# Optimization experiments

Measured on AMD Instinct MI355X. Metric: run time of the kernel, lower is better.

## Reference

```python
import jax, jax.numpy as jnp
import numpy as np

T, N, E = 336, 3233, 20000
FEAT, D, H = 14, 64, 128


def setup_inputs() -> dict:
    key = jax.random.key(0)
    ks = jax.random.split(key, 12)
    s = lambda k, shape, fan: jax.random.normal(k, shape, jnp.float32) / np.sqrt(fan)
    return {
        "x": jax.random.normal(ks[0], (T, N, FEAT), jnp.float32),
        "edge_index": jax.random.randint(ks[1], (2, E), 0, N, jnp.int64 if jax.config.jax_enable_x64 else jnp.int32),
        "edge_weight": jax.random.uniform(ks[2], (E,), jnp.float32),
        "W1": s(ks[3], (FEAT, D), FEAT), "b1": jnp.zeros((D,), jnp.float32),
        "W2": s(ks[4], (D, D), D), "b2": jnp.zeros((D,), jnp.float32),
        "county_bias": s(ks[5], (N, D), D),
        "W_ih": s(ks[6], (4 * H, D), D), "W_hh": s(ks[7], (4 * H, H), H),
        "b_ih": jnp.zeros((4 * H,), jnp.float32), "b_hh": jnp.zeros((4 * H,), jnp.float32),
        "Wm1": s(ks[8], (H, H // 2), H), "bm1": jnp.zeros((H // 2,), jnp.float32),
        "Wm2": s(ks[9], (H // 2, 1), H // 2), "bm2": jnp.zeros((1,), jnp.float32),
    }


def _gcn_norm(edge_index, edge_weight, n):
    # PyG GCNConv: add self-loops (weight 1) + symmetric normalization
    loop = jnp.arange(n, dtype=edge_index.dtype)
    src = jnp.concatenate([edge_index[0], loop])
    dst = jnp.concatenate([edge_index[1], loop])
    w = jnp.concatenate([edge_weight, jnp.ones((n,), edge_weight.dtype)])
    deg = jax.ops.segment_sum(w, dst, num_segments=n)
    dis = jnp.where(deg > 0, jax.lax.rsqrt(jnp.where(deg > 0, deg, 1.0)), 0.0)
    return src, dst, dis[src] * w * dis[dst]


def _gcn(h, src, dst, norm, W, b):
    # h: [T,N,Fin] -> [T,N,Fout]; transform then gather-scale-scatter over edges
    hw = jnp.einsum("tnf,fd->tnd", h, W)
    msg = hw[:, src, :] * norm[None, :, None]          # [T,E',Fout]
    out = jnp.zeros_like(hw).at[:, dst, :].add(msg)
    return out + b


def reference(x, edge_index, edge_weight, W1, b1, W2, b2, county_bias,
              W_ih, W_hh, b_ih, b_hh, Wm1, bm1, Wm2, bm2):
    n = x.shape[1]
    src, dst, norm = _gcn_norm(edge_index, edge_weight, n)
    h = jax.nn.relu(_gcn(x, src, dst, norm, W1, b1))
    embeds = _gcn(h, src, dst, norm, W2, b2) + county_bias[None]  # [T,N,D]

    hid = W_hh.shape[1]
    def step(carry, x_t):  # x_t: [N,D]
        hprev, cprev = carry
        g = x_t @ W_ih.T + hprev @ W_hh.T + (b_ih + b_hh)
        i, f, gg, o = jnp.split(g, 4, axis=-1)
        c = jax.nn.sigmoid(f) * cprev + jax.nn.sigmoid(i) * jnp.tanh(gg)
        hh = jax.nn.sigmoid(o) * jnp.tanh(c)
        return (hh, c), None

    init = (jnp.zeros((n, hid), x.dtype), jnp.zeros((n, hid), x.dtype))
    (h_final, _), _ = jax.lax.scan(step, init, embeds)
    z = jax.nn.relu(h_final @ Wm1 + bm1)
    return (z @ Wm2 + bm2)[:, 0]
```

## Files before the change

### kernel.cpp

```cpp
#include <hip/hip_runtime.h>
#include <math.h>


#define T_DIM 336
#define N_DIM 3233
#define E_DIM 20000
#define FEAT  14
#define D_DIM 64
#define H_DIM 128
#define ET    (E_DIM + N_DIM)

typedef _Float16 f16;
typedef _Float16 half8_t __attribute__((ext_vector_type(8)));
typedef float float4_t __attribute__((ext_vector_type(4)));

__device__ __forceinline__ float sigf(float x) {
    return __builtin_amdgcn_rcpf(1.f + exp2f(-1.4426950408889634f * x));
}
__device__ __forceinline__ float tanhfast(float x) {
    return 1.f - 2.f * __builtin_amdgcn_rcpf(1.f + exp2f(2.8853900817779268f * x));
}


__global__ void k_init(int* cnt, int* fill) {
    int i = blockIdx.x * 256 + threadIdx.x;
    if (i < N_DIM) { cnt[i] = 0; fill[i] = 0; }
}

__global__ void k_cnt(const int* __restrict__ ei, int* cnt) {
    int e = blockIdx.x * 256 + threadIdx.x;
    if (e < E_DIM) atomicAdd(&cnt[ei[E_DIM + e]], 1);
}

__global__ void k_scan(const int* __restrict__ cnt, int* __restrict__ rowp) {
    __shared__ int csum[1024];
    int tid = threadIdx.x;
    int base = tid * 4;
    int v[4];
    int s = 0;
    #pragma unroll
    for (int m = 0; m < 4; m++) {
        int idx = base + m;
        int len = (idx < N_DIM) ? (cnt[idx] + 1) : 0;
        v[m] = s; s += len;
    }
    csum[tid] = s;
    __syncthreads();
    for (int off = 1; off < 1024; off <<= 1) {
        int t2 = (tid >= off) ? csum[tid - off] : 0;
        __syncthreads();
        csum[tid] += t2;
        __syncthreads();
    }
    int pre = (tid > 0) ? csum[tid - 1] : 0;
    #pragma unroll
    for (int m = 0; m < 4; m++) {
        int idx = base + m;
        if (idx <= N_DIM) rowp[idx] = pre + v[m];
    }
}

__global__ void k_fill(const int* __restrict__ ei, const int* __restrict__ rowp,
                       int* fill, int* __restrict__ eid) {
    int e = blockIdx.x * 256 + threadIdx.x;
    if (e < ET) {
        int d = (e < E_DIM) ? ei[E_DIM + e] : (e - E_DIM);
        int p = rowp[d] + atomicAdd(&fill[d], 1);
        eid[p] = e;
    }
}

__global__ void k_sortdeg(const float* __restrict__ ew, const int* __restrict__ rowp,
                          int* __restrict__ eid, float* __restrict__ dis) {
    int n = blockIdx.x * 256 + threadIdx.x;
    if (n >= N_DIM) return;
    int p0 = rowp[n], p1 = rowp[n + 1];
    for (int i = p0 + 1; i < p1; i++) {
        int key = eid[i];
        int j = i - 1;
        while (j >= p0 && eid[j] > key) { eid[j + 1] = eid[j]; j--; }
        eid[j + 1] = key;
    }
    float deg = 0.f;
    for (int p = p0; p < p1; p++) {
        int e = eid[p];
        deg += (e < E_DIM) ? ew[e] : 1.0f;
    }
    dis[n] = rsqrtf(deg);
}

__global__ void k_csrmat(const int* __restrict__ ei, const float* __restrict__ ew,
                         const float* __restrict__ dis, const int* __restrict__ rowp,
                         const int* __restrict__ eid, int* __restrict__ csrc,
                         float* __restrict__ cnrm) {
    int n = blockIdx.x * 256 + threadIdx.x;
    if (n >= N_DIM) return;
    float dn = dis[n];
    int p0 = rowp[n], p1 = rowp[n + 1];
    for (int p = p0; p < p1; p++) {
        int e = eid[p];
        int s; float w;
        if (e < E_DIM) { s = ei[e]; w = ew[e]; }
        else           { s = e - E_DIM; w = 1.0f; }
        csrc[p] = s;
        cnrm[p] = dis[s] * w * dn;
    }
}

__global__ void k_wprep(const float* __restrict__ W2, const float* __restrict__ Wih,
                        const float* __restrict__ Whh, f16* __restrict__ wfbuf) {
    int idx = blockIdx.x * 256 + threadIdx.x;
    if (idx >= 8 * 4 * 6 * 64) return;
    int lane = idx & 63;
    int ks = (idx >> 6) % 6;
    int ct = ((idx >> 6) / 6) & 3;
    int wv = (idx >> 6) / 24;
    int q = lane >> 4, r = lane & 15;
    int g = 128 * ct + 16 * wv + r;
    f16* dst = wfbuf + (long)idx * 8;
    if (ks < 2) {
        const float* wir = Wih + (long)g * 64;
        #pragma unroll
        for (int j = 0; j < 8; j++) {
            int k = 32 * ks + 8 * q + j;
            const float* w2r = W2 + (long)k * 64;
            float s = 0.f;
            #pragma unroll 16
            for (int d = 0; d < 64; d++) s += w2r[d] * wir[d];
            dst[j] = (f16)s;
        }
    } else {
        const float* src = Whh + (long)g * 128 + 32 * (ks - 2) + 8 * q;
        #pragma unroll
        for (int j = 0; j < 8; j++) dst[j] = (f16)src[j];
    }
}

__global__ void k_gbias(const float* __restrict__ county, const float* __restrict__ b2,
                        const float* __restrict__ Wih, const float* __restrict__ bih,
                        const float* __restrict__ bhh, float* __restrict__ gbias) {
    long id = (long)blockIdx.x * 256 + threadIdx.x;
    if (id >= (long)N_DIM * 512) return;
    int n = (int)(id >> 9), g = (int)(id & 511);
    const float* wir = Wih + (long)g * 64;
    const float* cn = county + (long)n * 64;
    float s = bih[g] + bhh[g];
    #pragma unroll 16
    for (int d = 0; d < 64; d++) s += (b2[d] + cn[d]) * wir[d];
    gbias[id] = s;
}

__global__ void k_aggx(const float* __restrict__ x, const int* __restrict__ rowp,
                       const int* __restrict__ csrc, const float* __restrict__ cnrm,
                       float* __restrict__ aggX, int tc) {
    int lane = threadIdx.x & 63;
    long wid = ((long)blockIdx.x * 256 + threadIdx.x) >> 6;
    int ntg = (tc + 3) >> 2;
    if (wid >= (long)N_DIM * ntg) return;
    int n = (int)(wid % N_DIM);
    int tg = (int)(wid / N_DIM);
    int j = lane >> 4, d = lane & 15;
    int tj = 4 * tg + j;
    bool live = (d < FEAT) && (tj < tc);
    float acc = 0.f;
    int p0 = rowp[n], p1 = rowp[n + 1];
    for (int p = p0; p < p1; p++) {
        int s = csrc[p];
        float w = cnrm[p];
        if (live) acc += w * x[((long)tj * N_DIM + s) * FEAT + d];
    }
    if (tj < tc) aggX[((long)tj * N_DIM + n) * 16 + d] = acc;
}

__global__ void k_tr1(const float* __restrict__ aggX, const float* __restrict__ W1,
                      const float* __restrict__ b1, f16* __restrict__ h, long rows) {
    int lane = threadIdx.x & 63;
    long wid = ((long)blockIdx.x * 256 + threadIdx.x) >> 6;
    float wc[FEAT];
    #pragma unroll
    for (int k = 0; k < FEAT; k++) wc[k] = W1[k * 64 + lane];
    float bb = b1[lane];
    long r0 = wid * 2;
    if (r0 >= rows) return;
    long r1 = r0 + 1;
    bool has1 = (r1 < rows);
    const float* p0 = aggX + r0 * 16;
    const float* p1 = aggX + (has1 ? r1 : r0) * 16;
    float a0 = bb, a1 = bb;
    #pragma unroll
    for (int k = 0; k < FEAT; k++) { a0 += p0[k] * wc[k]; a1 += p1[k] * wc[k]; }
    h[r0 * 64 + lane] = (f16)fmaxf(a0, 0.f);
    if (has1) h[r1 * 64 + lane] = (f16)fmaxf(a1, 0.f);
}

__global__ void k_agg2(const f16* __restrict__ h, const int* __restrict__ rowp,
                       const int* __restrict__ csrc, const float* __restrict__ cnrm,
                       f16* __restrict__ ah, int tc) {
    int lane = threadIdx.x & 63;
    long wid = ((long)blockIdx.x * 256 + threadIdx.x) >> 6;
    int ntg = (tc + 3) >> 2;
    if (wid >= (long)N_DIM * ntg) return;
    int n = (int)(wid % N_DIM);
    int tg = (int)(wid / N_DIM);
    int tbase = 4 * tg;
    float acc0 = 0.f, acc1 = 0.f, acc2 = 0.f, acc3 = 0.f;
    int p0 = rowp[n], p1 = rowp[n + 1];
    for (int p = p0; p < p1; p++) {
        int s = csrc[p];
        float w = cnrm[p];
        const f16* base = h + ((long)tbase * N_DIM + s) * 64 + lane;
        acc0 += w * (float)base[0];
        if (tbase + 1 < tc) acc1 += w * (float)base[(long)N_DIM * 64];
        if (tbase + 2 < tc) acc2 += w * (float)base[(long)N_DIM * 128];
        if (tbase + 3 < tc) acc3 += w * (float)base[(long)N_DIM * 192];
    }
    f16* dst = ah + ((long)tbase * N_DIM + n) * 64 + lane;
    dst[0] = (f16)acc0;
    if (tbase + 1 < tc) dst[(long)N_DIM * 64] = (f16)acc1;
    if (tbase + 2 < tc) dst[(long)N_DIM * 128] = (f16)acc2;
    if (tbase + 3 < tc) dst[(long)N_DIM * 192] = (f16)acc3;
}

__global__ __attribute__((amdgpu_flat_work_group_size(512, 512), amdgpu_waves_per_eu(2, 2)))
void k_lstm(
    const f16* __restrict__ ah, const f16* __restrict__ wfbuf,
    const float* __restrict__ gbias,
    const float* __restrict__ Wm1, const float* __restrict__ bm1,
    const float* __restrict__ Wm2, const float* __restrict__ bm2,
    float* __restrict__ Hst, float* __restrict__ Cst,
    int tc, int do_init, int do_head, float* __restrict__ out) {
    __shared__ __align__(16) f16   xh[2][16][136];
    __shared__ __align__(16) float hd[16][132];
    __shared__ __align__(16) float zs[16][64];

    int tid = threadIdx.x;
    int wv = tid >> 6, lane = tid & 63, q = lane >> 4, r = lane & 15;
    int nb = blockIdx.x * 16;
    int cnt = min(16, N_DIM - nb);
    int u = 16 * wv + r;

    float4_t wfr[4][6];
    #pragma unroll
    for (int ct = 0; ct < 4; ct++)
        #pragma unroll
        for (int ks = 0; ks < 6; ks++)
            wfr[ct][ks] = *(const float4_t*)&wfbuf[(long)((((wv * 4 + ct) * 6 + ks) << 6) + lane) * 8];
    #pragma unroll
    for (int ct = 0; ct < 4; ct++)
        #pragma unroll
        for (int ks = 0; ks < 6; ks++)
            asm volatile("" : "+v"(wfr[ct][ks]));

    float gb[4][4];
    #pragma unroll
    for (int reg = 0; reg < 4; reg++) {
        int node = 4 * q + reg;
        int gn = nb + node; if (gn >= N_DIM) gn = N_DIM - 1;
        #pragma unroll
        for (int ct = 0; ct < 4; ct++)
            gb[ct][reg] = gbias[(long)gn * 512 + 128 * ct + u];
    }
    #pragma unroll
    for (int ct = 0; ct < 4; ct++)
        #pragma unroll
        for (int reg = 0; reg < 4; reg++)
            asm volatile("" : "+v"(gb[ct][reg]));

    float cv[4], hvv[4];
    #pragma unroll
    for (int reg = 0; reg < 4; reg++) {
        int node = 4 * q + reg;
        bool live = (!do_init) && (node < cnt);
        hvv[reg] = live ? Hst[(long)(nb + node) * H_DIM + u] : 0.f;
        cv[reg]  = live ? Cst[(long)(nb + node) * H_DIM + u] : 0.f;
        xh[0][node][u] = (f16)hvv[reg];
    }

    int xrow = nb + r; if (xrow >= N_DIM) xrow = N_DIM - 1;
    half8_t xa = *(const half8_t*)(ah + (long)xrow * 64 + 8 * q);
    half8_t xb = *(const half8_t*)(ah + (long)xrow * 64 + 32 + 8 * q);

    int buf = 0;
    __syncthreads();

    for (int t = 0; t < tc; t++) {
        half8_t a2 = *(const half8_t*)&xh[buf][r][8 * q];
        half8_t a3 = *(const half8_t*)&xh[buf][r][32 + 8 * q];
        half8_t a4 = *(const half8_t*)&xh[buf][r][64 + 8 * q];
        half8_t a5 = *(const half8_t*)&xh[buf][r][96 + 8 * q];

        float4_t acc[4];
        #pragma unroll
        for (int ct = 0; ct < 4; ct++) {
            acc[ct][0] = gb[ct][0]; acc[ct][1] = gb[ct][1];
            acc[ct][2] = gb[ct][2]; acc[ct][3] = gb[ct][3];
        }
        #pragma unroll
        for (int ct = 0; ct < 4; ct++)
            acc[ct] = __builtin_amdgcn_mfma_f32_16x16x32_f16(xa, __builtin_bit_cast(half8_t, wfr[ct][0]), acc[ct], 0, 0, 0);
        #pragma unroll
        for (int ct = 0; ct < 4; ct++)
            acc[ct] = __builtin_amdgcn_mfma_f32_16x16x32_f16(xb, __builtin_bit_cast(half8_t, wfr[ct][1]), acc[ct], 0, 0, 0);

        int tn = (t + 1 < tc) ? t + 1 : t;
        const f16* xp = ah + ((long)tn * N_DIM + xrow) * 64;
        xa = *(const half8_t*)(xp + 8 * q);
        xb = *(const half8_t*)(xp + 32 + 8 * q);

        #pragma unroll
        for (int ct = 0; ct < 4; ct++)
            acc[ct] = __builtin_amdgcn_mfma_f32_16x16x32_f16(a2, __builtin_bit_cast(half8_t, wfr[ct][2]), acc[ct], 0, 0, 0);
        #pragma unroll
        for (int ct = 0; ct < 4; ct++)
            acc[ct] = __builtin_amdgcn_mfma_f32_16x16x32_f16(a3, __builtin_bit_cast(half8_t, wfr[ct][3]), acc[ct], 0, 0, 0);
        #pragma unroll
        for (int ct = 0; ct < 4; ct++)
            acc[ct] = __builtin_amdgcn_mfma_f32_16x16x32_f16(a4, __builtin_bit_cast(half8_t, wfr[ct][4]), acc[ct], 0, 0, 0);
        #pragma unroll
        for (int ct = 0; ct < 4; ct++)
            acc[ct] = __builtin_amdgcn_mfma_f32_16x16x32_f16(a5, __builtin_bit_cast(half8_t, wfr[ct][5]), acc[ct], 0, 0, 0);

        #pragma unroll
        for (int reg = 0; reg < 4; reg++) {
            float gi = acc[0][reg], gf = acc[1][reg], gg = acc[2][reg], go = acc[3][reg];
            float c = sigf(gf) * cv[reg] + sigf(gi) * tanhfast(gg);
            float hh = sigf(go) * tanhfast(c);
            cv[reg] = c; hvv[reg] = hh;
            xh[buf ^ 1][4 * q + reg][u] = (f16)hh;
        }
        __syncthreads();
        buf ^= 1;
    }

    #pragma unroll
    for (int reg = 0; reg < 4; reg++) {
        int node = 4 * q + reg;
        if (node < cnt) {
            Hst[(long)(nb + node) * H_DIM + u] = hvv[reg];
            Cst[(long)(nb + node) * H_DIM + u] = cv[reg];
        }
    }
    if (!do_head) return;

    #pragma unroll
    for (int reg = 0; reg < 4; reg++) hd[4 * q + reg][u] = hvv[reg];
    __syncthreads();

    for (int i = tid; i < 16 * 64; i += 512) {
        int n = i >> 6, m = i & 63;
        float a = bm1[m];
        #pragma unroll 8
        for (int k = 0; k < H_DIM; k++) a += hd[n][k] * Wm1[k * 64 + m];
        zs[n][m] = fmaxf(a, 0.f);
    }
    __syncthreads();
    if (tid < cnt) {
        float a = bm2[0];
        #pragma unroll 8
        for (int m = 0; m < 64; m++) a += zs[tid][m] * Wm2[m];
        out[nb + tid] = a;
    }
}


extern "C" void kernel_launch(void* const* d_in, const int* in_sizes, int n_in,
                              void* d_out, int out_size, void* d_ws, size_t ws_size,
                              hipStream_t stream) {
    const float* x   = (const float*)d_in[0];
    const int*   ei  = (const int*)d_in[1];
    const float* ew  = (const float*)d_in[2];
    const float* W1  = (const float*)d_in[3];
    const float* b1  = (const float*)d_in[4];
    const float* W2  = (const float*)d_in[5];
    const float* b2  = (const float*)d_in[6];
    const float* cb  = (const float*)d_in[7];
    const float* Wih = (const float*)d_in[8];
    const float* Whh = (const float*)d_in[9];
    const float* bih = (const float*)d_in[10];
    const float* bhh = (const float*)d_in[11];
    const float* Wm1 = (const float*)d_in[12];
    const float* bm1 = (const float*)d_in[13];
    const float* Wm2 = (const float*)d_in[14];
    const float* bm2 = (const float*)d_in[15];
    float* out = (float*)d_out;
    (void)in_sizes; (void)n_in; (void)out_size;

    char* ws = (char*)d_ws;
    size_t off = 0;
    auto alloc = [&](size_t bytes) -> char* {
        char* p = ws + off;
        off = (off + bytes + 255) & ~(size_t)255;
        return p;
    };
    float* dis   = (float*)alloc(N_DIM * 4);
    int*   cnt   = (int*)alloc(N_DIM * 4);
    int*   fill  = (int*)alloc(N_DIM * 4);
    int*   rowp  = (int*)alloc((N_DIM + 1) * 4);
    int*   eid   = (int*)alloc(ET * 4);
    int*   csrc  = (int*)alloc(ET * 4);
    float* cnrm  = (float*)alloc(ET * 4);
    float* Hst   = (float*)alloc((size_t)N_DIM * H_DIM * 4);
    float* Cst   = (float*)alloc((size_t)N_DIM * H_DIM * 4);
    f16*   wfbuf = (f16*)alloc((size_t)8 * 4 * 6 * 64 * 8 * 2);
    float* gbias = (float*)alloc((size_t)N_DIM * 512 * 4);

    const int cand[] = {336, 168, 112, 84, 56, 48, 28, 16, 8, 4};
    int Tc = 4;
    for (int i = 0; i < 10; i++) {
        size_t need = off + (size_t)cand[i] * N_DIM * 320 + 4096;
        if (need <= ws_size) { Tc = cand[i]; break; }
    }
    long rows = (long)Tc * N_DIM;
    float* aggX  = (float*)alloc(rows * 64);
    f16*   hbuf  = (f16*)alloc(rows * 128);
    f16*   ahbuf = (f16*)alloc(rows * 128);

    k_init<<<(N_DIM + 255) / 256, 256, 0, stream>>>(cnt, fill);
    k_cnt<<<(E_DIM + 255) / 256, 256, 0, stream>>>(ei, cnt);
    k_scan<<<1, 1024, 0, stream>>>(cnt, rowp);
    k_fill<<<(ET + 255) / 256, 256, 0, stream>>>(ei, rowp, fill, eid);
    k_sortdeg<<<(N_DIM + 255) / 256, 256, 0, stream>>>(ew, rowp, eid, dis);
    k_csrmat<<<(N_DIM + 255) / 256, 256, 0, stream>>>(ei, ew, dis, rowp, eid, csrc, cnrm);
    k_wprep<<<48, 256, 0, stream>>>(W2, Wih, Whh, wfbuf);
    k_gbias<<<(int)(((long)N_DIM * 512 + 255) / 256), 256, 0, stream>>>(cb, b2, Wih, bih, bhh, gbias);

    int ntg = (Tc + 3) >> 2;
    long aggWaves = (long)N_DIM * ntg;
    int aggBlocks = (int)((aggWaves + 3) / 4);
    int trBlocks  = (int)(((rows + 1) / 2 + 3) / 4);
    int lblocks   = (N_DIM + 15) / 16;
    int nChunks   = T_DIM / Tc;

    for (int c = 0; c < nChunks; c++) {
        long t0 = (long)c * Tc;
        k_aggx<<<aggBlocks, 256, 0, stream>>>(x + t0 * N_DIM * FEAT, rowp, csrc, cnrm, aggX, Tc);
        k_tr1<<<trBlocks, 256, 0, stream>>>(aggX, W1, b1, hbuf, rows);
        k_agg2<<<aggBlocks, 256, 0, stream>>>(hbuf, rowp, csrc, cnrm, ahbuf, Tc);
        k_lstm<<<lblocks, 512, 0, stream>>>(ahbuf, wfbuf, gbias, Wm1, bm1, Wm2, bm2,
                                            Hst, Cst, Tc, c == 0 ? 1 : 0,
                                            c == nChunks - 1 ? 1 : 0, out);
    }
}
```

Before: 1.305 ms.

## Split LSTM step K-reduction across two wave groups with LDS exchange

New measurement: 1.419 ms. +8.7%, slower.

```diff
diff --git a/kernel.cpp b/kernel.cpp
--- a/kernel.cpp
+++ b/kernel.cpp
@@ -9,6 +9,13 @@
 #define D_DIM 64
 #define H_DIM 128
 #define ET    (E_DIM + N_DIM)
+
+#define L_XH   0
+#define L_EX   8704
+#define L_GB   (8704 + 32768)
+#define L_HD   8704
+#define L_ZS   (8704 + 8448)
+#define LDS_TOTAL (8704 + 32768 + 32768)
 
 typedef _Float16 f16;
 typedef _Float16 half8_t __attribute__((ext_vector_type(8)));
@@ -221,133 +228,145 @@
     if (tbase + 3 < tc) dst[(long)N_DIM * 192] = (f16)acc3;
 }
 
-__global__ __attribute__((amdgpu_flat_work_group_size(512, 512), amdgpu_waves_per_eu(2, 2)))
-void k_lstm(
+__global__ __launch_bounds__(1024, 1) void k_lstm(
     const f16* __restrict__ ah, const f16* __restrict__ wfbuf,
     const float* __restrict__ gbias,
     const float* __restrict__ Wm1, const float* __restrict__ bm1,
     const float* __restrict__ Wm2, const float* __restrict__ bm2,
     float* __restrict__ Hst, float* __restrict__ Cst,
     int tc, int do_init, int do_head, float* __restrict__ out) {
-    __shared__ __align__(16) f16   xh[2][16][136];
-    __shared__ __align__(16) float hd[16][132];
-    __shared__ __align__(16) float zs[16][64];
+    extern __shared__ __align__(16) char smem[];
+    f16 (*xh)[16][136] = (f16(*)[16][136])(smem + L_XH);
+    float* ex = (float*)(smem + L_EX);
+    float* gb = (float*)(smem + L_GB);
+    float (*hd)[132] = (float(*)[132])(smem + L_HD);
+    float (*zs)[64]  = (float(*)[64])(smem + L_ZS);
 
     int tid = threadIdx.x;
-    int wv = tid >> 6, lane = tid & 63, q = lane >> 4, r = lane & 15;
+    int grp = tid >> 9;
+    int wv = (tid >> 6) & 7;
+    int lane = tid & 63, q = lane >> 4, r = lane & 15;
     int nb = blockIdx.x * 16;
     int cnt = min(16, N_DIM - nb);
     int u = 16 * wv + r;
 
-    float4_t wfr[4][6];
+    half8_t wf[4][3];
     #pragma unroll
     for (int ct = 0; ct < 4; ct++)
         #pragma unroll
-        for (int ks = 0; ks < 6; ks++)
-            wfr[ct][ks] = *(const float4_t*)&wfbuf[(long)((((wv * 4 + ct) * 6 + ks) << 6) + lane) * 8];
-    #pragma unroll
-    for (int ct = 0; ct < 4; ct++)
-        #pragma unroll
-        for (int ks = 0; ks < 6; ks++)
-            asm volatile("" : "+v"(wfr[ct][ks]));
-
-    float gb[4][4];
-    #pragma unroll
-    for (int reg = 0; reg < 4; reg++) {
-        int node = 4 * q + reg;
-        int gn = nb + node; if (gn >= N_DIM) gn = N_DIM - 1;
-        #pragma unroll
-        for (int ct = 0; ct < 4; ct++)
-            gb[ct][reg] = gbias[(long)gn * 512 + 128 * ct + u];
-    }
-    #pragma unroll
-    for (int ct = 0; ct < 4; ct++)
-        #pragma unroll
-        for (int reg = 0; reg < 4; reg++)
-            asm volatile("" : "+v"(gb[ct][reg]));
+        for (int j = 0; j < 3; j++) {
+            int ks = grp * 3 + j;
+            wf[ct][j] = *(const half8_t*)&wfbuf[(long)((((wv * 4 + ct) * 6 + ks) << 6) + lane) * 8];
+        }
 
     float cv[4], hvv[4];
-    #pragma unroll
-    for (int reg = 0; reg < 4; reg++) {
-        int node = 4 * q + reg;
-        bool live = (!do_init) && (node < cnt);
-        hvv[reg] = live ? Hst[(long)(nb + node) * H_DIM + u] : 0.f;
-        cv[reg]  = live ? Cst[(long)(nb + node) * H_DIM + u] : 0.f;
-        xh[0][node][u] = (f16)hvv[reg];
-    }
-
+    half8_t xa, xb;
     int xrow = nb + r; if (xrow >= N_DIM) xrow = N_DIM - 1;
-    half8_t xa = *(const half8_t*)(ah + (long)xrow * 64 + 8 * q);
-    half8_t xb = *(const half8_t*)(ah + (long)xrow * 64 + 32 + 8 * q);
+    if (!grp) {
+        #pragma unroll
+        for (int ct = 0; ct < 4; ct++) {
+            #pragma unroll
+            for (int reg = 0; reg < 4; reg++) {
+                int gn = nb + 4 * q + reg; if (gn >= N_DIM) gn = N_DIM - 1;
+                gb[(((wv * 4 + ct) << 6) + lane) * 4 + reg] =
+                    gbias[(long)gn * 512 + 128 * ct + u];
+            }
+        }
+        #pragma unroll
+        for (int reg = 0; reg < 4; reg++) {
+            int node = 4 * q + reg;
+            bool live = (!do_init) && (node < cnt);
+            hvv[reg] = live ? Hst[(long)(nb + node) * H_DIM + u] : 0.f;
+            cv[reg]  = live ? Cst[(long)(nb + node) * H_DIM + u] : 0.f;
+            xh[0][node][u] = (f16)hvv[reg];
+        }
+        xa = *(const half8_t*)(ah + (long)xrow * 64 + 8 * q);
+        xb = *(const half8_t*)(ah + (long)xrow * 64 + 32 + 8 * q);
+    }
 
     int buf = 0;
     __syncthreads();
 
     for (int t = 0; t < tc; t++) {
-        half8_t a2 = *(const half8_t*)&xh[buf][r][8 * q];
-        half8_t a3 = *(const half8_t*)&xh[buf][r][32 + 8 * q];
-        half8_t a4 = *(const half8_t*)&xh[buf][r][64 + 8 * q];
-        half8_t a5 = *(const half8_t*)&xh[buf][r][96 + 8 * q];
-
         float4_t acc[4];
-        #pragma unroll
-        for (int ct = 0; ct < 4; ct++) {
-            acc[ct][0] = gb[ct][0]; acc[ct][1] = gb[ct][1];
-            acc[ct][2] = gb[ct][2]; acc[ct][3] = gb[ct][3];
-        }
-        #pragma unroll
-        for (int ct = 0; ct < 4; ct++)
-            acc[ct] = __builtin_amdgcn_mfma_f32_16x16x32_f16(xa, __builtin_bit_cast(half8_t, wfr[ct][0]), acc[ct], 0, 0, 0);
-        #pragma unroll
-        for (int ct = 0; ct < 4; ct++)
-            acc[ct] = __builtin_amdgcn_mfma_f32_16x16x32_f16(xb, __builtin_bit_cast(half8_t, wfr[ct][1]), acc[ct], 0, 0, 0);
-
-        int tn = (t + 1 < tc) ? t + 1 : t;
-        const f16* xp = ah + ((long)tn * N_DIM + xrow) * 64;
-        xa = *(const half8_t*)(xp + 8 * q);
-        xb = *(const half8_t*)(xp + 32 + 8 * q);
-
-        #pragma unroll
-        for (int ct = 0; ct < 4; ct++)
-            acc[ct] = __builtin_amdgcn_mfma_f32_16x16x32_f16(a2, __builtin_bit_cast(half8_t, wfr[ct][2]), acc[ct], 0, 0, 0);
-        #pragma unroll
-        for (int ct = 0; ct < 4; ct++)
-            acc[ct] = __builtin_amdgcn_mfma_f32_16x16x32_f16(a3, __builtin_bit_cast(half8_t, wfr[ct][3]), acc[ct], 0, 0, 0);
-        #pragma unroll
-        for (int ct = 0; ct < 4; ct++)
-            acc[ct] = __builtin_amdgcn_mfma_f32_16x16x32_f16(a4, __builtin_bit_cast(half8_t, wfr[ct][4]), acc[ct], 0, 0, 0);
-        #pragma unroll
-        for (int ct = 0; ct < 4; ct++)
-            acc[ct] = __builtin_amdgcn_mfma_f32_16x16x32_f16(a5, __builtin_bit_cast(half8_t, wfr[ct][5]), acc[ct], 0, 0, 0);
-
-        #pragma unroll
-        for (int reg = 0; reg < 4; reg++) {
-            float gi = acc[0][reg], gf = acc[1][reg], gg = acc[2][reg], go = acc[3][reg];
-            float c = sigf(gf) * cv[reg] + sigf(gi) * tanhfast(gg);
-            float hh = sigf(go) * tanhfast(c);
-            cv[reg] = c; hvv[reg] = hh;
-            xh[buf ^ 1][4 * q + reg][u] = (f16)hh;
+        if (!grp) {
+            half8_t a2 = *(const half8_t*)&xh[buf][r][8 * q];
+            #pragma unroll
+            for (int ct = 0; ct < 4; ct++)
+                acc[ct] = *(const float4_t*)&gb[(((wv * 4 + ct) << 6) + lane) * 4];
+            #pragma unroll
+            for (int ct = 0; ct < 4; ct++)
+                acc[ct] = __builtin_amdgcn_mfma_f32_16x16x32_f16(xa, wf[ct][0], acc[ct], 0, 0, 0);
+            #pragma unroll
+            for (int ct = 0; ct < 4; ct++)
+                acc[ct] = __builtin_amdgcn_mfma_f32_16x16x32_f16(xb, wf[ct][1], acc[ct], 0, 0, 0);
+            int tn = (t + 1 < tc) ? t + 1 : t;
+            const f16* xp = ah + ((long)tn * N_DIM + xrow) * 64;
+            xa = *(const half8_t*)(xp + 8 * q);
+            xb = *(const half8_t*)(xp + 32 + 8 * q);
+            #pragma unroll
+            for (int ct = 0; ct < 4; ct++)
+                acc[ct] = __builtin_amdgcn_mfma_f32_16x16x32_f16(a2, wf[ct][2], acc[ct], 0, 0, 0);
+        } else {
+            half8_t a3 = *(const half8_t*)&xh[buf][r][32 + 8 * q];
+            half8_t a4 = *(const half8_t*)&xh[buf][r][64 + 8 * q];
+            half8_t a5 = *(const half8_t*)&xh[buf][r][96 + 8 * q];
+            #pragma unroll
+            for (int ct = 0; ct < 4; ct++) acc[ct] = (float4_t){0.f, 0.f, 0.f, 0.f};
+            #pragma unroll
+            for (int ct = 0; ct < 4; ct++)
+                acc[ct] = __builtin_amdgcn_mfma_f32_16x16x32_f16(a3, wf[ct][0], acc[ct], 0, 0, 0);
+            #pragma unroll
+            for (int ct = 0; ct < 4; ct++)
+                acc[ct] = __builtin_amdgcn_mfma_f32_16x16x32_f16(a4, wf[ct][1], acc[ct], 0, 0, 0);
+            #pragma unroll
+            for (int ct = 0; ct < 4; ct++)
+                acc[ct] = __builtin_amdgcn_mfma_f32_16x16x32_f16(a5, wf[ct][2], acc[ct], 0, 0, 0);
+            #pragma unroll
+            for (int ct = 0; ct < 4; ct++)
+                *(float4_t*)&ex[(((wv * 4 + ct) << 6) + lane) * 4] = acc[ct];
+        }
+        __syncthreads();
+
+        if (!grp) {
+            #pragma unroll
+            for (int ct = 0; ct < 4; ct++) {
+                float4_t e = *(const float4_t*)&ex[(((wv * 4 + ct) << 6) + lane) * 4];
+                acc[ct] += e;
+            }
+            #pragma unroll
+            for (int reg = 0; reg < 4; reg++) {
+                float gi = acc[0][reg], gf = acc[1][reg], gg = acc[2][reg], go = acc[3][reg];
+                float c = sigf(gf) * cv[reg] + sigf(gi) * tanhfast(gg);
+                float hh = sigf(go) * tanhfast(c);
+                cv[reg] = c; hvv[reg] = hh;
+                xh[buf ^ 1][4 * q + reg][u] = (f16)hh;
+            }
         }
         __syncthreads();
         buf ^= 1;
     }
 
-    #pragma unroll
-    for (int reg = 0; reg < 4; reg++) {
-        int node = 4 * q + reg;
-        if (node < cnt) {
-            Hst[(long)(nb + node) * H_DIM + u] = hvv[reg];
-            Cst[(long)(nb + node) * H_DIM + u] = cv[reg];
+    if (!grp) {
+        #pragma unroll
+        for (int reg = 0; reg < 4; reg++) {
+            int node = 4 * q + reg;
+            if (node < cnt) {
+                Hst[(long)(nb + node) * H_DIM + u] = hvv[reg];
+                Cst[(long)(nb + node) * H_DIM + u] = cv[reg];
+            }
         }
     }
     if (!do_head) return;
 
-    #pragma unroll
-    for (int reg = 0; reg < 4; reg++) hd[4 * q + reg][u] = hvv[reg];
+    if (!grp) {
+        #pragma unroll
+        for (int reg = 0; reg < 4; reg++) hd[4 * q + reg][u] = hvv[reg];
+    }
     __syncthreads();
 
-    for (int i = tid; i < 16 * 64; i += 512) {
-        int n = i >> 6, m = i & 63;
+    {
+        int n = tid >> 6, m = tid & 63;
         float a = bm1[m];
         #pragma unroll 8
         for (int k = 0; k < H_DIM; k++) a += hd[n][k] * Wm1[k * 64 + m];
@@ -385,6 +404,9 @@
     float* out = (float*)d_out;
     (void)in_sizes; (void)n_in; (void)out_size;
 
+    hipFuncSetAttribute((const void*)k_lstm,
+                        hipFuncAttributeMaxDynamicSharedMemorySize, LDS_TOTAL);
+
     char* ws = (char*)d_ws;
     size_t off = 0;
     auto alloc = [&](size_t bytes) -> char* {
@@ -436,8 +458,8 @@
         k_aggx<<<aggBlocks, 256, 0, stream>>>(x + t0 * N_DIM * FEAT, rowp, csrc, cnrm, aggX, Tc);
         k_tr1<<<trBlocks, 256, 0, stream>>>(aggX, W1, b1, hbuf, rows);
         k_agg2<<<aggBlocks, 256, 0, stream>>>(hbuf, rowp, csrc, cnrm, ahbuf, Tc);
-        k_lstm<<<lblocks, 512, 0, stream>>>(ahbuf, wfbuf, gbias, Wm1, bm1, Wm2, bm2,
-                                            Hst, Cst, Tc, c == 0 ? 1 : 0,
-                                            c == nChunks - 1 ? 1 : 0, out);
-    }
-}
+        k_lstm<<<lblocks, 1024, LDS_TOTAL, stream>>>(ahbuf, wfbuf, gbias, Wm1, bm1, Wm2, bm2,
+                                                     Hst, Cst, Tc, c == 0 ? 1 : 0,
+                                                     c == nChunks - 1 ? 1 : 0, out);
+    }
+}
```
